# Performance work log

Measured on AMD Instinct MI355X. Metric: run time of the kernel, lower is better.

## Reference

```python
import jax, jax.numpy as jnp
import numpy as np

N_NODES = 100000
N_EDGES = 3200000
D = 64
H = D * D  # GRU hidden size 4096


def _gru_cell(x, h, W_ih, W_hh, b_ih, b_hh):
    # torch.nn.GRUCell math; x, h are 1-D [H]
    gi = W_ih @ x + b_ih  # [3H]
    gh = W_hh @ h + b_hh  # [3H]
    i_r, i_z, i_n = jnp.split(gi, 3)
    h_r, h_z, h_n = jnp.split(gh, 3)
    r = jax.nn.sigmoid(i_r + h_r)
    z = jax.nn.sigmoid(i_z + h_z)
    n = jnp.tanh(i_n + r * h_n)
    return (1.0 - z) * n + z * h


def _gcn_layer(x, src, dst, W, b, out_norm, in_norm, activation=None):
    # DGL GraphConv with norm='both': D_out^{-1/2} -> aggregate -> D_in^{-1/2} -> XW + b
    x = x * out_norm[:, None]
    msg = x[src]  # gather over edges [E, D]
    agg = jax.ops.segment_sum(msg, dst, num_segments=N_NODES)
    agg = agg * in_norm[:, None]
    h = agg @ W + b
    if activation is not None:
        h = activation(h)
    return h


def setup_inputs() -> dict:
    key = jax.random.key(0)
    ks = jax.random.split(key, 10)
    node_embeddings = jax.random.normal(ks[0], (N_NODES, D), jnp.float32)
    gc1_weight = jax.random.normal(ks[1], (D, D), jnp.float32) * 0.1
    gc2_weight = jax.random.normal(ks[2], (D, D), jnp.float32) * 0.1
    gc1_bias = jnp.zeros((D,), jnp.float32)
    gc2_bias = jnp.zeros((D,), jnp.float32)
    prev_gc1 = jax.random.normal(ks[3], (H,), jnp.float32) * 0.1
    prev_gc2 = jax.random.normal(ks[4], (H,), jnp.float32) * 0.1
    W_ih = jax.random.normal(ks[5], (3 * H, H), jnp.float32) * 0.02
    W_hh = jax.random.normal(ks[6], (3 * H, H), jnp.float32) * 0.02
    b_ih = jnp.zeros((3 * H,), jnp.float32)
    b_hh = jnp.zeros((3 * H,), jnp.float32)
    src = jax.random.randint(ks[7], (N_EDGES,), 0, N_NODES, jnp.int32)
    dst = jax.random.randint(ks[8], (N_EDGES,), 0, N_NODES, jnp.int32)
    return {
        "node_embeddings": node_embeddings,
        "gc1_weight": gc1_weight, "gc2_weight": gc2_weight,
        "gc1_bias": gc1_bias, "gc2_bias": gc2_bias,
        "prev_gc1": prev_gc1, "prev_gc2": prev_gc2,
        "W_ih": W_ih, "W_hh": W_hh, "b_ih": b_ih, "b_hh": b_hh,
        "src": src, "dst": dst,
    }


def reference(node_embeddings, gc1_weight, gc2_weight, gc1_bias, gc2_bias,
              prev_gc1, prev_gc2, W_ih, W_hh, b_ih, b_hh, src, dst):
    ones = jnp.ones((N_EDGES,), jnp.float32)
    out_deg = jax.ops.segment_sum(ones, src, num_segments=N_NODES)
    in_deg = jax.ops.segment_sum(ones, dst, num_segments=N_NODES)
    out_norm = jax.lax.rsqrt(jnp.maximum(out_deg, 1.0))
    in_norm = jax.lax.rsqrt(jnp.maximum(in_deg, 1.0))

    # weight evolution: GRUCell(input=prev weights, hidden=current flat weights)
    w1 = _gru_cell(prev_gc1, gc1_weight.reshape(-1), W_ih, W_hh, b_ih, b_hh).reshape(D, D)
    w2 = _gru_cell(prev_gc2, gc2_weight.reshape(-1), W_ih, W_hh, b_ih, b_hh).reshape(D, D)

    h = _gcn_layer(node_embeddings, src, dst, w1, gc1_bias, out_norm, in_norm,
                   activation=jax.nn.relu)
    h = _gcn_layer(h, src, dst, w2, gc2_bias, out_norm, in_norm, activation=None)
    return h
```

## Files before the change

### kernel.cpp

```cpp
#include <hip/hip_runtime.h>
#include <math.h>

#define NN 100000
#define NE 3200000
#define D 64
#define H 4096
#define H3 12288

#define NBKT 782
#define NBKTP 784
#define PCHUNK 4096
#define NPART 782
#define CAP 8192

__global__ __launch_bounds__(256) void hist_kernel(const int* __restrict__ src,
                                                   const int* __restrict__ dst,
                                                   int* __restrict__ outcnt,
                                                   int* __restrict__ bucketCnt) {
    __shared__ int h[NBKT];
    for (int i = threadIdx.x; i < NBKT; i += 256) h[i] = 0;
    __syncthreads();
    int stride = gridDim.x * 256;
    for (int e = blockIdx.x * 256 + threadIdx.x; e < NE; e += stride) {
        int d = dst[e];
        atomicAdd(&h[d >> 7], 1);
        atomicAdd(&outcnt[src[e]], 1);
    }
    __syncthreads();
    for (int i = threadIdx.x; i < NBKT; i += 256)
        if (h[i]) atomicAdd(&bucketCnt[i], h[i]);
}

__global__ __launch_bounds__(1024) void bucket_scan(const int* __restrict__ bucketCnt,
                                                    int* __restrict__ bucketPtr,
                                                    int* __restrict__ bucketCur,
                                                    int* __restrict__ rowptr) {
    __shared__ int s[1024];
    int t = threadIdx.x;
    int v = (t < NBKT) ? bucketCnt[t] : 0;
    s[t] = v;
    __syncthreads();
    for (int off = 1; off < 1024; off <<= 1) {
        int u = (t >= off) ? s[t - off] : 0;
        __syncthreads();
        s[t] += u;
        __syncthreads();
    }
    int excl = s[t] - v;
    if (t < NBKT) { bucketPtr[t] = excl; bucketCur[t] = excl; }
    if (t == 0)   { bucketPtr[NBKT] = NE; rowptr[NN] = NE; }
}

__global__ __launch_bounds__(256) void partition_kernel(const int* __restrict__ src,
                                                        const int* __restrict__ dst,
                                                        int* __restrict__ bucketCur,
                                                        int* __restrict__ recs) {
    __shared__ int h[NBKTP];
    __shared__ int st[NBKTP];
    __shared__ int shf[NBKTP];
    __shared__ int ss[256];
    __shared__ unsigned stage[PCHUNK];
    __shared__ unsigned short bos[PCHUNK];

    int t = threadIdx.x;
    for (int i = t; i < NBKTP; i += 256) h[i] = 0;
    __syncthreads();

    int e0 = blockIdx.x * PCHUNK;
    int n = NE - e0; if (n > PCHUNK) n = PCHUNK;

    for (int i = t; i < n; i += 256) atomicAdd(&h[dst[e0 + i] >> 7], 1);
    __syncthreads();

    int c0 = 0, c1 = 0, c2 = 0, c3 = 0, sum = 0;
    int b4 = t * 4;
    if (b4 < NBKTP)     { c0 = h[b4];     sum += c0; }
    if (b4 + 1 < NBKTP) { c1 = h[b4 + 1]; sum += c1; }
    if (b4 + 2 < NBKTP) { c2 = h[b4 + 2]; sum += c2; }
    if (b4 + 3 < NBKTP) { c3 = h[b4 + 3]; sum += c3; }
    ss[t] = sum;
    __syncthreads();
    for (int off = 1; off < 256; off <<= 1) {
        int u = (t >= off) ? ss[t - off] : 0;
        __syncthreads();
        ss[t] += u;
        __syncthreads();
    }
    int run = ss[t] - sum;
    if (b4 < NBKTP)     { st[b4]     = run; run += c0; }
    if (b4 + 1 < NBKTP) { st[b4 + 1] = run; run += c1; }
    if (b4 + 2 < NBKTP) { st[b4 + 2] = run; run += c2; }
    if (b4 + 3 < NBKTP) { st[b4 + 3] = run; run += c3; }
    __syncthreads();

    for (int b = t; b < NBKT; b += 256) {
        int cc = h[b];
        if (cc) {
            int g = atomicAdd(&bucketCur[b], cc);
            shf[b] = g - st[b];
        }
    }
    __syncthreads();

    for (int i = t; i < n; i += 256) {
        int d = dst[e0 + i];
        int b = d >> 7;
        int slot = atomicAdd(&st[b], 1);
        stage[slot] = ((unsigned)src[e0 + i] << 7) | (unsigned)(d & 127);
        bos[slot] = (unsigned short)b;
    }
    __syncthreads();

    for (int s2 = t; s2 < n; s2 += 256)
        recs[shf[bos[s2]] + s2] = (int)stage[s2];
}

__global__ __launch_bounds__(256) void bucket_csr(int* __restrict__ recs,
                                                  const int* __restrict__ bucketPtr,
                                                  int* __restrict__ rowptr,
                                                  float* __restrict__ innorm) {
    __shared__ int h[128];
    __shared__ int pex[128];
    __shared__ int stageS[CAP];
    int b = blockIdx.x, t = threadIdx.x;
    int p0 = bucketPtr[b], p1 = bucketPtr[b + 1];
    int cnt = p1 - p0;
    if (cnt > CAP) cnt = CAP;
    if (t < 128) h[t] = 0;
    __syncthreads();

    for (int i = t; i < cnt; i += 256) {
        int r = recs[p0 + i];
        stageS[i] = r;
        atomicAdd(&h[r & 127], 1);
    }
    __syncthreads();

    if (t < 128) pex[t] = h[t];
    __syncthreads();
    for (int off = 1; off < 128; off <<= 1) {
        int u = 0;
        if (t < 128 && t >= off) u = pex[t - off];
        __syncthreads();
        if (t < 128) pex[t] += u;
        __syncthreads();
    }
    if (t < 128) {
        int ex = pex[t] - h[t];
        int node = b * 128 + t;
        if (node < NN) {
            rowptr[node] = p0 + ex;
            innorm[node] = rsqrtf(fmaxf((float)h[t], 1.0f));
        }
        pex[t] = ex;
    }
    __syncthreads();

    for (int i = t; i < cnt; i += 256) {
        int r = stageS[i];
        int slot = atomicAdd(&pex[r & 127], 1);
        recs[p0 + slot] = r >> 7;
    }
}

__global__ __launch_bounds__(256) void outnorm_kernel(const int* __restrict__ outcnt,
                                                      float* __restrict__ outn) {
    int i = blockIdx.x * 256 + threadIdx.x;
    if (i < NN) outn[i] = rsqrtf(fmaxf((float)outcnt[i], 1.0f));
}

__global__ __launch_bounds__(256) void gru_matvec(
    const float* __restrict__ Wih, const float* __restrict__ Whh,
    const float* __restrict__ bih, const float* __restrict__ bhh,
    const float* __restrict__ pg1, const float* __restrict__ pg2,
    const float* __restrict__ g1w, const float* __restrict__ g2w,
    float* __restrict__ gi1, float* __restrict__ gh1,
    float* __restrict__ gi2, float* __restrict__ gh2) {
    int r = blockIdx.x;
    int tid = threadIdx.x;
    const float4* wi = (const float4*)(Wih + (size_t)r * H);
    const float4* wh = (const float4*)(Whh + (size_t)r * H);
    const float4* x1 = (const float4*)pg1;
    const float4* x2 = (const float4*)pg2;
    const float4* h1 = (const float4*)g1w;
    const float4* h2 = (const float4*)g2w;
    float a0 = 0.f, a1 = 0.f, a2 = 0.f, a3 = 0.f;
    for (int k = tid; k < H / 4; k += 256) {
        float4 wiv = wi[k];
        float4 whv = wh[k];
        float4 v1 = x1[k], v2 = x2[k], u1 = h1[k], u2 = h2[k];
        a0 += wiv.x * v1.x + wiv.y * v1.y + wiv.z * v1.z + wiv.w * v1.w;
        a1 += whv.x * u1.x + whv.y * u1.y + whv.z * u1.z + whv.w * u1.w;
        a2 += wiv.x * v2.x + wiv.y * v2.y + wiv.z * v2.z + wiv.w * v2.w;
        a3 += whv.x * u2.x + whv.y * u2.y + whv.z * u2.z + whv.w * u2.w;
    }
    for (int off = 32; off; off >>= 1) {
        a0 += __shfl_down(a0, off);
        a1 += __shfl_down(a1, off);
        a2 += __shfl_down(a2, off);
        a3 += __shfl_down(a3, off);
    }
    __shared__ float red[4][4];
    int wv = tid >> 6;
    if ((tid & 63) == 0) {
        red[wv][0] = a0; red[wv][1] = a1; red[wv][2] = a2; red[wv][3] = a3;
    }
    __syncthreads();
    if (tid < 4) {
        float s = red[0][tid] + red[1][tid] + red[2][tid] + red[3][tid];
        if (tid == 0)      gi1[r] = s + bih[r];
        else if (tid == 1) gh1[r] = s + bhh[r];
        else if (tid == 2) gi2[r] = s + bih[r];
        else               gh2[r] = s + bhh[r];
    }
}

__global__ __launch_bounds__(256) void gru_combine(
    const float* __restrict__ gi1, const float* __restrict__ gh1,
    const float* __restrict__ gi2, const float* __restrict__ gh2,
    const float* __restrict__ g1w, const float* __restrict__ g2w,
    float* __restrict__ w1, float* __restrict__ w2) {
    int gid = blockIdx.x * 256 + threadIdx.x;
    if (gid >= 2 * H) return;
    int c = gid >> 12;
    int j = gid & (H - 1);
    const float* gi = c ? gi2 : gi1;
    const float* gh = c ? gh2 : gh1;
    float hprev = c ? g2w[j] : g1w[j];
    float r = 1.f / (1.f + expf(-(gi[j] + gh[j])));
    float z = 1.f / (1.f + expf(-(gi[H + j] + gh[H + j])));
    float n = tanhf(gi[2 * H + j] + r * gh[2 * H + j]);
    float w = (1.f - z) * n + z * hprev;
    (c ? w2 : w1)[j] = w;
}

__global__ __launch_bounds__(256) void agg_gemm_fused(
    const int* __restrict__ rowptr, const int* __restrict__ csr_src,
    const float* __restrict__ x, const float* __restrict__ outn,
    const float* __restrict__ innorm, const float* __restrict__ W,
    const float* __restrict__ bias, float* __restrict__ out, int relu) {
    __shared__ float sW[D * D];
    int tid = threadIdx.x;
    for (int i = tid; i < D * D; i += 256) sW[i] = W[i];
    __syncthreads();
    int node = blockIdx.x * 4 + (tid >> 6);
    int lane = tid & 63;
    if (node >= NN) return;
    int e = rowptr[node], end = rowptr[node + 1];
    float acc = 0.f;
    for (; e + 3 < end; e += 4) {
        int s0 = csr_src[e], s1 = csr_src[e + 1];
        int s2 = csr_src[e + 2], s3 = csr_src[e + 3];
        float on0 = outn[s0], on1 = outn[s1], on2 = outn[s2], on3 = outn[s3];
        float v0 = x[(size_t)s0 * D + lane];
        float v1 = x[(size_t)s1 * D + lane];
        float v2 = x[(size_t)s2 * D + lane];
        float v3 = x[(size_t)s3 * D + lane];
        acc += v0 * on0 + v1 * on1 + v2 * on2 + v3 * on3;
    }
    for (; e < end; ++e) {
        int s0 = csr_src[e];
        acc += x[(size_t)s0 * D + lane] * outn[s0];
    }
    acc *= innorm[node];
    float o = 0.f;
#pragma unroll
    for (int k = 0; k < D; ++k) {
        float ak = __shfl(acc, k);
        o += ak * sW[k * D + lane];
    }
    o += bias[lane];
    if (relu) o = fmaxf(o, 0.f);
    out[(size_t)node * D + lane] = o;
}

extern "C" void kernel_launch(void* const* d_in, const int* in_sizes, int n_in,
                              void* d_out, int out_size, void* d_ws, size_t ws_size,
                              hipStream_t stream) {
    const float* x0   = (const float*)d_in[0];
    const float* gc1w = (const float*)d_in[1];
    const float* gc2w = (const float*)d_in[2];
    const float* gc1b = (const float*)d_in[3];
    const float* gc2b = (const float*)d_in[4];
    const float* pg1  = (const float*)d_in[5];
    const float* pg2  = (const float*)d_in[6];
    const float* Wih  = (const float*)d_in[7];
    const float* Whh  = (const float*)d_in[8];
    const float* bih  = (const float*)d_in[9];
    const float* bhh  = (const float*)d_in[10];
    const int*   src  = (const int*)d_in[11];
    const int*   dst  = (const int*)d_in[12];
    float* out = (float*)d_out;
    float* ws  = (float*)d_ws;

    float* outn     = ws;
    float* innorm   = ws + 100000;
    int* outcnt     = (int*)(ws + 200000);
    int* bucketCnt  = (int*)(ws + 300000);
    int* bucketPtr  = (int*)(ws + 301024);
    int* bucketCur  = (int*)(ws + 302048);
    int* rowptr     = (int*)(ws + 303072);
    float* w1  = ws + 403104;
    float* w2  = ws + 407200;
    float* gi1 = ws + 411296;
    float* gh1 = ws + 423584;
    float* gi2 = ws + 435872;
    float* gh2 = ws + 448160;
    int* csr   = (int*)(ws + 460448);
    float* h1w = ws + 3660448;

    hipMemsetAsync(outcnt, 0, (size_t)(100000 + 1024) * sizeof(int), stream);

    hist_kernel<<<2048, 256, 0, stream>>>(src, dst, outcnt, bucketCnt);
    bucket_scan<<<1, 1024, 0, stream>>>(bucketCnt, bucketPtr, bucketCur, rowptr);
    partition_kernel<<<NPART, 256, 0, stream>>>(src, dst, bucketCur, csr);
    bucket_csr<<<NBKT, 256, 0, stream>>>(csr, bucketPtr, rowptr, innorm);
    outnorm_kernel<<<(NN + 255) / 256, 256, 0, stream>>>(outcnt, outn);

    gru_matvec<<<H3, 256, 0, stream>>>(Wih, Whh, bih, bhh, pg1, pg2, gc1w, gc2w,
                                       gi1, gh1, gi2, gh2);
    gru_combine<<<(2 * H + 255) / 256, 256, 0, stream>>>(gi1, gh1, gi2, gh2,
                                                         gc1w, gc2w, w1, w2);

    agg_gemm_fused<<<(NN + 3) / 4, 256, 0, stream>>>(rowptr, csr, x0, outn,
                                                     innorm, w1, gc1b, h1w, 1);
    agg_gemm_fused<<<(NN + 3) / 4, 256, 0, stream>>>(rowptr, csr, h1w, outn,
                                                     innorm, w2, gc2b, out, 0);
}
```

Before: 1.043 ms.

## Fuse out-degree counting into partition, prescale layer-1 output, coalesce edge index loads

Out-degree counting moves from the histogram kernel into the partition kernel, and the out-norm computation moves into bucket_csr, which removes one kernel and a redundant pass over src. The first GCN layer now multiplies its output by the next layer's out-norm, so the second layer skips the per-edge outn gather. The aggregation loop loads 64 edge indices cooperatively, one per lane, broadcasts them with shuffles, and unrolls the feature gathers by 8 for more memory-level parallelism. The cost is extra shuffle instructions and more register use per edge batch.

```diff
diff --git a/kernel.cpp b/kernel.cpp
--- a/kernel.cpp
+++ b/kernel.cpp
@@ -13,19 +13,14 @@
 #define NPART 782
 #define CAP 8192
 
-__global__ __launch_bounds__(256) void hist_kernel(const int* __restrict__ src,
-                                                   const int* __restrict__ dst,
-                                                   int* __restrict__ outcnt,
+__global__ __launch_bounds__(256) void hist_kernel(const int* __restrict__ dst,
                                                    int* __restrict__ bucketCnt) {
     __shared__ int h[NBKT];
     for (int i = threadIdx.x; i < NBKT; i += 256) h[i] = 0;
     __syncthreads();
     int stride = gridDim.x * 256;
-    for (int e = blockIdx.x * 256 + threadIdx.x; e < NE; e += stride) {
-        int d = dst[e];
-        atomicAdd(&h[d >> 7], 1);
-        atomicAdd(&outcnt[src[e]], 1);
-    }
+    for (int e = blockIdx.x * 256 + threadIdx.x; e < NE; e += stride)
+        atomicAdd(&h[dst[e] >> 7], 1);
     __syncthreads();
     for (int i = threadIdx.x; i < NBKT; i += 256)
         if (h[i]) atomicAdd(&bucketCnt[i], h[i]);
@@ -54,6 +49,7 @@
 __global__ __launch_bounds__(256) void partition_kernel(const int* __restrict__ src,
                                                         const int* __restrict__ dst,
                                                         int* __restrict__ bucketCur,
+                                                        int* __restrict__ outcnt,
                                                         int* __restrict__ recs) {
     __shared__ int h[NBKTP];
     __shared__ int st[NBKTP];
@@ -69,7 +65,10 @@
     int e0 = blockIdx.x * PCHUNK;
     int n = NE - e0; if (n > PCHUNK) n = PCHUNK;
 
-    for (int i = t; i < n; i += 256) atomicAdd(&h[dst[e0 + i] >> 7], 1);
+    for (int i = t; i < n; i += 256) {
+        atomicAdd(&h[dst[e0 + i] >> 7], 1);
+        atomicAdd(&outcnt[src[e0 + i]], 1);
+    }
     __syncthreads();
 
     int c0 = 0, c1 = 0, c2 = 0, c3 = 0, sum = 0;
@@ -117,8 +116,10 @@
 
 __global__ __launch_bounds__(256) void bucket_csr(int* __restrict__ recs,
                                                   const int* __restrict__ bucketPtr,
+                                                  const int* __restrict__ outcnt,
                                                   int* __restrict__ rowptr,
-                                                  float* __restrict__ innorm) {
+                                                  float* __restrict__ innorm,
+                                                  float* __restrict__ outn) {
     __shared__ int h[128];
     __shared__ int pex[128];
     __shared__ int stageS[CAP];
@@ -151,6 +152,7 @@
         if (node < NN) {
             rowptr[node] = p0 + ex;
             innorm[node] = rsqrtf(fmaxf((float)h[t], 1.0f));
+            outn[node]   = rsqrtf(fmaxf((float)outcnt[node], 1.0f));
         }
         pex[t] = ex;
     }
@@ -161,12 +163,6 @@
         int slot = atomicAdd(&pex[r & 127], 1);
         recs[p0 + slot] = r >> 7;
     }
-}
-
-__global__ __launch_bounds__(256) void outnorm_kernel(const int* __restrict__ outcnt,
-                                                      float* __restrict__ outn) {
-    int i = blockIdx.x * 256 + threadIdx.x;
-    if (i < NN) outn[i] = rsqrtf(fmaxf((float)outcnt[i], 1.0f));
 }
 
 __global__ __launch_bounds__(256) void gru_matvec(
@@ -234,11 +230,13 @@
     (c ? w2 : w1)[j] = w;
 }
 
+template <int USE_ON>
 __global__ __launch_bounds__(256) void agg_gemm_fused(
     const int* __restrict__ rowptr, const int* __restrict__ csr_src,
     const float* __restrict__ x, const float* __restrict__ outn,
     const float* __restrict__ innorm, const float* __restrict__ W,
-    const float* __restrict__ bias, float* __restrict__ out, int relu) {
+    const float* __restrict__ bias, const float* __restrict__ outn_next,
+    float* __restrict__ out, int relu) {
     __shared__ float sW[D * D];
     int tid = threadIdx.x;
     for (int i = tid; i < D * D; i += 256) sW[i] = W[i];
@@ -246,31 +244,45 @@
     int node = blockIdx.x * 4 + (tid >> 6);
     int lane = tid & 63;
     if (node >= NN) return;
-    int e = rowptr[node], end = rowptr[node + 1];
+    int e0 = rowptr[node], e1 = rowptr[node + 1];
     float acc = 0.f;
-    for (; e + 3 < end; e += 4) {
-        int s0 = csr_src[e], s1 = csr_src[e + 1];
-        int s2 = csr_src[e + 2], s3 = csr_src[e + 3];
-        float on0 = outn[s0], on1 = outn[s1], on2 = outn[s2], on3 = outn[s3];
-        float v0 = x[(size_t)s0 * D + lane];
-        float v1 = x[(size_t)s1 * D + lane];
-        float v2 = x[(size_t)s2 * D + lane];
-        float v3 = x[(size_t)s3 * D + lane];
-        acc += v0 * on0 + v1 * on1 + v2 * on2 + v3 * on3;
-    }
-    for (; e < end; ++e) {
-        int s0 = csr_src[e];
-        acc += x[(size_t)s0 * D + lane] * outn[s0];
+    for (int base = e0; base < e1; base += 64) {
+        int nk = e1 - base; if (nk > 64) nk = 64;
+        int m = base + lane;
+        int idxv = (m < e1) ? csr_src[m] : 0;
+        float onv = 0.f;
+        if (USE_ON) onv = (m < e1) ? outn[idxv] : 0.f;
+        int k = 0;
+        for (; k + 8 <= nk; k += 8) {
+            int ss[8]; float oo[8]; float vv[8];
+#pragma unroll
+            for (int u = 0; u < 8; ++u) {
+                ss[u] = __shfl(idxv, k + u);
+                if (USE_ON) oo[u] = __shfl(onv, k + u);
+            }
+#pragma unroll
+            for (int u = 0; u < 8; ++u)
+                vv[u] = x[(size_t)ss[u] * D + lane];
+#pragma unroll
+            for (int u = 0; u < 8; ++u)
+                acc += USE_ON ? vv[u] * oo[u] : vv[u];
+        }
+        for (; k < nk; ++k) {
+            int s = __shfl(idxv, k);
+            float v = x[(size_t)s * D + lane];
+            acc += USE_ON ? v * __shfl(onv, k) : v;
+        }
     }
     acc *= innorm[node];
     float o = 0.f;
 #pragma unroll
-    for (int k = 0; k < D; ++k) {
-        float ak = __shfl(acc, k);
-        o += ak * sW[k * D + lane];
+    for (int kk = 0; kk < D; ++kk) {
+        float ak = __shfl(acc, kk);
+        o += ak * sW[kk * D + lane];
     }
     o += bias[lane];
     if (relu) o = fmaxf(o, 0.f);
+    if (outn_next) o *= outn_next[node];
     out[(size_t)node * D + lane] = o;
 }
 
@@ -307,23 +319,22 @@
     float* gi2 = ws + 435872;
     float* gh2 = ws + 448160;
     int* csr   = (int*)(ws + 460448);
-    float* h1w = ws + 3660448;
+    float* h1s = ws + 3660448;
 
     hipMemsetAsync(outcnt, 0, (size_t)(100000 + 1024) * sizeof(int), stream);
 
-    hist_kernel<<<2048, 256, 0, stream>>>(src, dst, outcnt, bucketCnt);
+    hist_kernel<<<2048, 256, 0, stream>>>(dst, bucketCnt);
     bucket_scan<<<1, 1024, 0, stream>>>(bucketCnt, bucketPtr, bucketCur, rowptr);
-    partition_kernel<<<NPART, 256, 0, stream>>>(src, dst, bucketCur, csr);
-    bucket_csr<<<NBKT, 256, 0, stream>>>(csr, bucketPtr, rowptr, innorm);
-    outnorm_kernel<<<(NN + 255) / 256, 256, 0, stream>>>(outcnt, outn);
+    partition_kernel<<<NPART, 256, 0, stream>>>(src, dst, bucketCur, outcnt, csr);
+    bucket_csr<<<NBKT, 256, 0, stream>>>(csr, bucketPtr, outcnt, rowptr, innorm, outn);
 
     gru_matvec<<<H3, 256, 0, stream>>>(Wih, Whh, bih, bhh, pg1, pg2, gc1w, gc2w,
                                        gi1, gh1, gi2, gh2);
     gru_combine<<<(2 * H + 255) / 256, 256, 0, stream>>>(gi1, gh1, gi2, gh2,
                                                          gc1w, gc2w, w1, w2);
 
-    agg_gemm_fused<<<(NN + 3) / 4, 256, 0, stream>>>(rowptr, csr, x0, outn,
-                                                     innorm, w1, gc1b, h1w, 1);
-    agg_gemm_fused<<<(NN + 3) / 4, 256, 0, stream>>>(rowptr, csr, h1w, outn,
-                                                     innorm, w2, gc2b, out, 0);
-}
+    agg_gemm_fused<1><<<(NN + 3) / 4, 256, 0, stream>>>(rowptr, csr, x0, outn,
+                                                        innorm, w1, gc1b, outn, h1s, 1);
+    agg_gemm_fused<0><<<(NN + 3) / 4, 256, 0, stream>>>(rowptr, csr, h1s, outn,
+                                                        innorm, w2, gc2b, nullptr, out, 0);
+}
```

Measured after the change: 998.5 us. 1.04x faster.
